# Optimization experiments

Measured on AMD Instinct MI355X. Metric: run time of the kernel, lower is better.

## Reference

```python
import jax, jax.numpy as jnp
import numpy as np

N = 100000   # nodes
E = 1600000  # edges
L = 3        # nlayers
H = 4        # nheads
DH = 32      # nhid (per-head)
F = 128      # nfeat == H*DH (residual-compatible)
NC = 1       # nclass
NEG = 0.2    # leaky relu negative slope (alpha)
EPS = 1e-5   # batchnorm eps


def gat_conv(x, src, dst, W, a_s, a_d, b, concat):
    """PyG-style GATConv (flow=source_to_target): softmax over incoming edges of dst."""
    n = x.shape[0]
    h = (x @ W).reshape(n, a_s.shape[0], a_s.shape[1])  # [N,H,Dh]
    s = jnp.einsum('nhd,hd->nh', h, a_s)  # score from source features
    d = jnp.einsum('nhd,hd->nh', h, a_d)  # score from target features
    e = jax.nn.leaky_relu(s[src] + d[dst], NEG)  # [E,H]
    m = jax.ops.segment_max(e, dst, num_segments=n)
    m = jnp.where(jnp.isfinite(m), m, 0.0)  # nodes with no in-edges
    p = jnp.exp(e - m[dst])
    z = jax.ops.segment_sum(p, dst, num_segments=n)
    alpha = p / (z[dst] + 1e-16)  # [E,H] segment softmax
    out = jax.ops.segment_sum(h[src] * alpha[:, :, None], dst, num_segments=n)  # [N,H,Dh]
    if concat:
        return out.reshape(n, -1) + b
    return out.mean(axis=1) + b


def setup_inputs() -> dict:
    key = jax.random.key(0)
    k = jax.random.split(key, 10)
    return {
        'x': jax.random.normal(k[0], (N, F), jnp.float32),
        'edge_index': jax.random.randint(k[1], (2, E), 0, N, jnp.int32),
        'W': jax.random.normal(k[2], (L, F, H * DH), jnp.float32) * 0.05,
        'att_src': jax.random.normal(k[3], (L, H, DH), jnp.float32) * 0.05,
        'att_dst': jax.random.normal(k[4], (L, H, DH), jnp.float32) * 0.05,
        'bias': jnp.zeros((L, H * DH), jnp.float32),
        'bn_gamma': jnp.ones((L, H * DH), jnp.float32),
        'bn_beta': jnp.zeros((L, H * DH), jnp.float32),
        'bn_mean': jnp.zeros((L, H * DH), jnp.float32),
        'bn_var': jnp.ones((L, H * DH), jnp.float32),
        'W_out': jax.random.normal(k[5], (H * DH, NC), jnp.float32) * 0.05,
        'att_src_out': jax.random.normal(k[6], (1, NC), jnp.float32) * 0.05,
        'att_dst_out': jax.random.normal(k[7], (1, NC), jnp.float32) * 0.05,
        'bias_out': jnp.zeros((NC,), jnp.float32),
    }


def reference(x, edge_index, W, att_src, att_dst, bias, bn_gamma, bn_beta,
              bn_mean, bn_var, W_out, att_src_out, att_dst_out, bias_out):
    src, dst = edge_index[0], edge_index[1]
    h = x  # eval mode: dropout is identity
    for l in range(L):
        res = h
        out = gat_conv(h, src, dst, W[l], att_src[l], att_dst[l], bias[l], concat=True)
        # BatchNorm1d (eval: running stats)
        out = bn_gamma[l] * (out - bn_mean[l]) * jax.lax.rsqrt(bn_var[l] + EPS) + bn_beta[l]
        if l > 0:
            out = out + res
        h = jax.nn.elu(out)
    return gat_conv(h, src, dst, W_out, att_src_out, att_dst_out, bias_out, concat=False)
```

## Files before the change

kernel.cpp:

```cpp
#include <hip/hip_runtime.h>
#include <math.h>

#define NN 100000
#define EE 1600000
#define HH 4
#define LREL 0.2f
#define BNEPS 1e-5f
#define LOG2E 1.4426950408889634f

__global__ void k_zero(int* __restrict__ p, int n) {
    int stride = gridDim.x * blockDim.x;
    for (int i = blockIdx.x * blockDim.x + threadIdx.x; i < n; i += stride) p[i] = 0;
}

__global__ void k_hist(const int* __restrict__ dst, int* __restrict__ deg) {
    int stride = gridDim.x * blockDim.x;
    for (int e = blockIdx.x * blockDim.x + threadIdx.x; e < EE; e += stride)
        atomicAdd(&deg[dst[e]], 1);
}

__global__ void k_scan1(const int* __restrict__ deg, int* __restrict__ rp, int* __restrict__ part) {
    __shared__ int sd[256];
    int i = blockIdx.x * 256 + threadIdx.x;
    int v = (i < NN) ? deg[i] : 0;
    sd[threadIdx.x] = v;
    __syncthreads();
    for (int o = 1; o < 256; o <<= 1) {
        int t = (threadIdx.x >= o) ? sd[threadIdx.x - o] : 0;
        __syncthreads();
        sd[threadIdx.x] += t;
        __syncthreads();
    }
    if (i < NN) rp[i + 1] = sd[threadIdx.x];
    if (threadIdx.x == 255) part[blockIdx.x] = sd[255];
}

__global__ void k_scan2(int* __restrict__ part, int nb) {
    __shared__ int sd[512];
    int v = (threadIdx.x < nb) ? part[threadIdx.x] : 0;
    sd[threadIdx.x] = v;
    __syncthreads();
    for (int o = 1; o < 512; o <<= 1) {
        int t = (threadIdx.x >= o) ? sd[threadIdx.x - o] : 0;
        __syncthreads();
        sd[threadIdx.x] += t;
        __syncthreads();
    }
    if (threadIdx.x < nb) part[threadIdx.x] = sd[threadIdx.x] - v;
}

__global__ void k_scan3(const int* __restrict__ deg, int* __restrict__ rp,
                        const int* __restrict__ part, int* __restrict__ cur) {
    int i = blockIdx.x * 256 + threadIdx.x;
    if (i < NN) {
        int incl = rp[i + 1] + part[blockIdx.x];
        rp[i + 1] = incl;
        cur[i] = incl - deg[i];
        if (i == 0) rp[0] = 0;
    }
}

__global__ void k_scatter(const int* __restrict__ src, const int* __restrict__ dst,
                          int* __restrict__ cur, int* __restrict__ csr) {
    int stride = gridDim.x * blockDim.x;
    for (int e = blockIdx.x * blockDim.x + threadIdx.x; e < EE; e += stride) {
        int p = atomicAdd(&cur[dst[e]], 1);
        csr[p] = src[e];
    }
}

__global__ void k_bnprep(const float* __restrict__ bias, const float* __restrict__ gam,
                         const float* __restrict__ bet, const float* __restrict__ mu,
                         const float* __restrict__ var, float* __restrict__ sc,
                         float* __restrict__ off) {
    int i = threadIdx.x;
    if (i < 384) {
        float rs = rsqrtf(var[i] + BNEPS);
        float s = gam[i] * rs;
        sc[i] = s;
        off[i] = (bias[i] - mu[i]) * s + bet[i];
    }
}

__device__ inline unsigned bf16rne(float f) {
    unsigned u = __float_as_uint(f);
    return (u + 0x7FFFu + ((u >> 16) & 1u)) >> 16;
}

__launch_bounds__(256)
__global__ void k_gemm(const float* __restrict__ x, const float* __restrict__ W,
                       const float* __restrict__ as_, const float* __restrict__ ad_,
                       unsigned* __restrict__ hpb, float* __restrict__ s_arr, float* __restrict__ d_arr) {
    __shared__ float wl[32][128];
    __shared__ float xt[32][68];
    int tid = threadIdx.x;
    int tr = tid >> 5, tc = tid & 31;
    int n0 = blockIdx.x * 64;
    float acc[8][4];
#pragma unroll
    for (int r = 0; r < 8; r++)
#pragma unroll
        for (int c = 0; c < 4; c++) acc[r][c] = 0.f;

    for (int kc = 0; kc < 4; kc++) {
        int k0 = kc * 32;
#pragma unroll
        for (int i = 0; i < 4; i++) {
            int idx = tid + i * 256;
            int r = idx >> 5, c4 = idx & 31;
            *(float4*)&wl[r][c4 * 4] = *(const float4*)&W[(k0 + r) * 128 + c4 * 4];
        }
#pragma unroll
        for (int i = 0; i < 2; i++) {
            int idx = tid + i * 256;
            int r = idx >> 3, c4 = idx & 7;
            int row = n0 + r;
            float4 v = make_float4(0.f, 0.f, 0.f, 0.f);
            if (row < NN) v = *(const float4*)&x[row * 128 + k0 + c4 * 4];
            xt[c4 * 4 + 0][r] = v.x;
            xt[c4 * 4 + 1][r] = v.y;
            xt[c4 * 4 + 2][r] = v.z;
            xt[c4 * 4 + 3][r] = v.w;
        }
        __syncthreads();
#pragma unroll 8
        for (int k = 0; k < 32; k++) {
            float4 w4 = *(float4*)&wl[k][tc * 4];
            float xv[8];
            *(float4*)&xv[0] = *(float4*)&xt[k][tr * 8];
            *(float4*)&xv[4] = *(float4*)&xt[k][tr * 8 + 4];
#pragma unroll
            for (int r = 0; r < 8; r++) {
                acc[r][0] = fmaf(xv[r], w4.x, acc[r][0]);
                acc[r][1] = fmaf(xv[r], w4.y, acc[r][1]);
                acc[r][2] = fmaf(xv[r], w4.z, acc[r][2]);
                acc[r][3] = fmaf(xv[r], w4.w, acc[r][3]);
            }
        }
        __syncthreads();
    }
    int head = tc >> 3;
    float4 a4 = *(const float4*)&as_[head * 32 + (tc & 7) * 4];
    float4 b4 = *(const float4*)&ad_[head * 32 + (tc & 7) * 4];
#pragma unroll
    for (int r = 0; r < 8; r++) {
        int row = n0 + tr * 8 + r;
        float sp = acc[r][0] * a4.x + acc[r][1] * a4.y + acc[r][2] * a4.z + acc[r][3] * a4.w;
        float dp = acc[r][0] * b4.x + acc[r][1] * b4.y + acc[r][2] * b4.z + acc[r][3] * b4.w;
        sp += __shfl_xor(sp, 1); sp += __shfl_xor(sp, 2); sp += __shfl_xor(sp, 4);
        dp += __shfl_xor(dp, 1); dp += __shfl_xor(dp, 2); dp += __shfl_xor(dp, 4);
        if (row < NN) {
            unsigned u0 = bf16rne(acc[r][0]) | (bf16rne(acc[r][1]) << 16);
            unsigned u1 = bf16rne(acc[r][2]) | (bf16rne(acc[r][3]) << 16);
            *(uint2*)&hpb[(size_t)row * 64 + tc * 2] = make_uint2(u0, u1);
            if ((tc & 7) == 0) {
                s_arr[row * HH + head] = sp * LOG2E;
                d_arr[row * HH + head] = dp * LOG2E;
            }
        }
    }
}

__launch_bounds__(256)
__global__ void k_agg(const unsigned* __restrict__ hpb, const float* __restrict__ s_arr,
                      const float* __restrict__ d_arr, const int* __restrict__ rp,
                      const int* __restrict__ csr, const float* __restrict__ scp,
                      const float* __restrict__ offp, const float* __restrict__ hin,
                      float* __restrict__ hout, int use_res) {
    int n = blockIdx.x * 4 + (threadIdx.x >> 6);
    if (n >= NN) return;
    int lane = threadIdx.x & 63;
    int c0 = lane * 2;
    int head = lane >> 4;
    float dn = d_arr[n * HH + head];
    int e0 = rp[n], e1 = rp[n + 1];
    e0 = __builtin_amdgcn_readfirstlane(e0);
    e1 = __builtin_amdgcn_readfirstlane(e1);
    float z = 0.f, a0 = 0.f, a1 = 0.f;
#pragma unroll 8
    for (int j = e0; j < e1; j++) {
        int sid = __builtin_amdgcn_readfirstlane(csr[j]);
        float sv = s_arr[sid * HH + head];
        unsigned u = hpb[(size_t)sid * 64 + lane];
        float e = sv + dn;
        e = fmaxf(e, LREL * e);
        float p = exp2f(e);
        float vx = __uint_as_float(u << 16);
        float vy = __uint_as_float(u & 0xFFFF0000u);
        z += p;
        a0 = fmaf(p, vx, a0);
        a1 = fmaf(p, vy, a1);
    }
    float inv = 1.f / (z + 1e-16f);
    float2 scv = *(const float2*)&scp[c0];
    float2 ofv = *(const float2*)&offp[c0];
    float o0 = fmaf(a0 * inv, scv.x, ofv.x);
    float o1 = fmaf(a1 * inv, scv.y, ofv.y);
    if (use_res) {
        float2 rr = *(const float2*)&hin[n * 128 + c0];
        o0 += rr.x;
        o1 += rr.y;
    }
    o0 = (o0 > 0.f) ? o0 : (__expf(o0) - 1.f);
    o1 = (o1 > 0.f) ? o1 : (__expf(o1) - 1.f);
    *(float2*)&hout[n * 128 + c0] = make_float2(o0, o1);
}

__global__ void k_gemm_out(const float* __restrict__ h, const float* __restrict__ Wo,
                           const float* __restrict__ aso, const float* __restrict__ ado,
                           float2* __restrict__ hos, float* __restrict__ dro) {
    int t = blockIdx.x * 256 + threadIdx.x;
    int n = t >> 2, li = t & 3;
    if (n >= NN) return;
    const float* xr = h + n * 128 + li * 32;
    const float* wr = Wo + li * 32;
    float acc = 0.f;
#pragma unroll
    for (int j = 0; j < 32; j += 4) {
        float4 a = *(const float4*)&xr[j];
        float4 b = *(const float4*)&wr[j];
        acc += a.x * b.x + a.y * b.y + a.z * b.z + a.w * b.w;
    }
    acc += __shfl_xor(acc, 1);
    acc += __shfl_xor(acc, 2);
    if (li == 0) {
        hos[n] = make_float2(acc, acc * aso[0] * LOG2E);
        dro[n] = acc * ado[0] * LOG2E;
    }
}

__global__ void k_agg_out(const float2* __restrict__ hos, const float* __restrict__ dro,
                          const int* __restrict__ rp, const int* __restrict__ csr,
                          const float* __restrict__ bo, float* __restrict__ out) {
    int t = blockIdx.x * 256 + threadIdx.x;
    int n = t >> 3, li = t & 7;
    if (n >= NN) return;
    float dn = dro[n];
    float z = 0.f, a = 0.f;
    int e0 = rp[n], e1 = rp[n + 1];
    for (int j = e0 + li; j < e1; j += 8) {
        int sid = csr[j];
        float2 hs = hos[sid];
        float e = hs.y + dn;
        e = fmaxf(e, LREL * e);
        float p = exp2f(e);
        z += p;
        a = fmaf(p, hs.x, a);
    }
    z += __shfl_xor(z, 1); z += __shfl_xor(z, 2); z += __shfl_xor(z, 4);
    a += __shfl_xor(a, 1); a += __shfl_xor(a, 2); a += __shfl_xor(a, 4);
    if (li == 0) out[n] = a / (z + 1e-16f) + bo[0];
}

extern "C" void kernel_launch(void* const* d_in, const int* in_sizes, int n_in,
                              void* d_out, int out_size, void* d_ws, size_t ws_size,
                              hipStream_t stream) {
    const float* x   = (const float*)d_in[0];
    const int*   ei  = (const int*)d_in[1];
    const float* W   = (const float*)d_in[2];
    const float* as_ = (const float*)d_in[3];
    const float* ad_ = (const float*)d_in[4];
    const float* bias = (const float*)d_in[5];
    const float* gam = (const float*)d_in[6];
    const float* bet = (const float*)d_in[7];
    const float* mu  = (const float*)d_in[8];
    const float* var = (const float*)d_in[9];
    const float* Wo  = (const float*)d_in[10];
    const float* aso = (const float*)d_in[11];
    const float* ado = (const float*)d_in[12];
    const float* bo  = (const float*)d_in[13];
    float* out = (float*)d_out;

    const int* src = ei;
    const int* dst = ei + EE;

    char* wsp = (char*)d_ws;
    size_t off = 0;
    auto alloc = [&](size_t bytes) {
        void* p = wsp + off;
        off += (bytes + 511) & ~(size_t)511;
        return p;
    };
    float* hA     = (float*)alloc((size_t)NN * 128 * 4);
    float* hB     = (float*)alloc((size_t)NN * 128 * 4);
    unsigned* hpb = (unsigned*)alloc((size_t)NN * 64 * 4);
    float* s_arr  = (float*)alloc((size_t)NN * HH * 4);
    float* d_arr  = (float*)alloc((size_t)NN * HH * 4);
    float2* hos   = (float2*)alloc((size_t)NN * 8);
    float* dro    = (float*)alloc((size_t)NN * 4);
    float* bnsc   = (float*)alloc(384 * 4);
    float* bnoff  = (float*)alloc(384 * 4);
    int* deg      = (int*)alloc((size_t)NN * 4);
    int* rp       = (int*)alloc((size_t)(NN + 1) * 4);
    int* cur      = (int*)alloc((size_t)NN * 4);
    int* part     = (int*)alloc(512 * 4);
    int* csr      = (int*)alloc((size_t)EE * 4);

    const int NB = (NN + 255) / 256;

    k_zero<<<512, 256, 0, stream>>>(deg, NN);
    k_hist<<<2048, 256, 0, stream>>>(dst, deg);
    k_scan1<<<NB, 256, 0, stream>>>(deg, rp, part);
    k_scan2<<<1, 512, 0, stream>>>(part, NB);
    k_scan3<<<NB, 256, 0, stream>>>(deg, rp, part, cur);
    k_scatter<<<2048, 256, 0, stream>>>(src, dst, cur, csr);
    k_bnprep<<<1, 384, 0, stream>>>(bias, gam, bet, mu, var, bnsc, bnoff);

    const float* hcur = x;
    const int GEMM_GRID = (NN + 63) / 64;
    const int AGG_GRID = (NN + 3) / 4;
    const int QGRID = (NN * 4 + 255) / 256;
    for (int l = 0; l < 3; l++) {
        k_gemm<<<GEMM_GRID, 256, 0, stream>>>(hcur, W + (size_t)l * 128 * 128,
                                              as_ + l * 128, ad_ + l * 128,
                                              hpb, s_arr, d_arr);
        float* hnext = (l == 1) ? hB : hA;
        k_agg<<<AGG_GRID, 256, 0, stream>>>(hpb, s_arr, d_arr, rp, csr,
                                            bnsc + l * 128, bnoff + l * 128,
                                            hcur, hnext, (l > 0) ? 1 : 0);
        hcur = hnext;
    }
    k_gemm_out<<<QGRID, 256, 0, stream>>>(hcur, Wo, aso, ado, hos, dro);
    k_agg_out<<<(NN * 8 + 255) / 256, 256, 0, stream>>>(hos, dro, rp, csr, bo, out);
}
```

Measured before the change: 848.6 us.

## Build CSR via two-level bucket partition instead of global atomic histogram and scatter

Replaces the per-node global-atomic degree histogram, three-kernel scan and atomic scatter with a bucketed counting sort. Edges are first binned into 512-node buckets using shared-memory histograms and partitioned into a temporary (src,dst) buffer. Each bucket is then sorted locally in shared memory to produce row pointers and CSR. This cuts contended global atomics and random writes, and makes CSR writes local to each bucket. The cost is an extra 8-byte-per-edge buffer pass, and in-bucket edge order becomes nondeterministic.

```diff
diff --git a/kernel.cpp b/kernel.cpp
--- a/kernel.cpp
+++ b/kernel.cpp
@@ -7,65 +7,101 @@
 #define LREL 0.2f
 #define BNEPS 1e-5f
 #define LOG2E 1.4426950408889634f
+#define NBUK 196
+#define PCH 4096
 
 __global__ void k_zero(int* __restrict__ p, int n) {
     int stride = gridDim.x * blockDim.x;
     for (int i = blockIdx.x * blockDim.x + threadIdx.x; i < n; i += stride) p[i] = 0;
 }
 
-__global__ void k_hist(const int* __restrict__ dst, int* __restrict__ deg) {
-    int stride = gridDim.x * blockDim.x;
-    for (int e = blockIdx.x * blockDim.x + threadIdx.x; e < EE; e += stride)
-        atomicAdd(&deg[dst[e]], 1);
-}
-
-__global__ void k_scan1(const int* __restrict__ deg, int* __restrict__ rp, int* __restrict__ part) {
+__global__ void k_bhist(const int* __restrict__ dst, int* __restrict__ bh) {
+    __shared__ int lh[NBUK];
+    int tid = threadIdx.x;
+    for (int i = tid; i < NBUK; i += 256) lh[i] = 0;
+    __syncthreads();
+    int stride = gridDim.x * 256;
+    for (int e = blockIdx.x * 256 + tid; e < EE; e += stride)
+        atomicAdd(&lh[dst[e] >> 9], 1);
+    __syncthreads();
+    for (int i = tid; i < NBUK; i += 256)
+        if (lh[i]) atomicAdd(&bh[i], lh[i]);
+}
+
+__global__ void k_bscan(const int* __restrict__ bh, int* __restrict__ bo, int* __restrict__ bcur) {
     __shared__ int sd[256];
-    int i = blockIdx.x * 256 + threadIdx.x;
-    int v = (i < NN) ? deg[i] : 0;
-    sd[threadIdx.x] = v;
+    int t = threadIdx.x;
+    int v = (t < NBUK) ? bh[t] : 0;
+    sd[t] = v;
     __syncthreads();
     for (int o = 1; o < 256; o <<= 1) {
-        int t = (threadIdx.x >= o) ? sd[threadIdx.x - o] : 0;
-        __syncthreads();
-        sd[threadIdx.x] += t;
-        __syncthreads();
-    }
-    if (i < NN) rp[i + 1] = sd[threadIdx.x];
-    if (threadIdx.x == 255) part[blockIdx.x] = sd[255];
-}
-
-__global__ void k_scan2(int* __restrict__ part, int nb) {
-    __shared__ int sd[512];
-    int v = (threadIdx.x < nb) ? part[threadIdx.x] : 0;
-    sd[threadIdx.x] = v;
-    __syncthreads();
-    for (int o = 1; o < 512; o <<= 1) {
-        int t = (threadIdx.x >= o) ? sd[threadIdx.x - o] : 0;
-        __syncthreads();
-        sd[threadIdx.x] += t;
-        __syncthreads();
-    }
-    if (threadIdx.x < nb) part[threadIdx.x] = sd[threadIdx.x] - v;
-}
-
-__global__ void k_scan3(const int* __restrict__ deg, int* __restrict__ rp,
-                        const int* __restrict__ part, int* __restrict__ cur) {
-    int i = blockIdx.x * 256 + threadIdx.x;
-    if (i < NN) {
-        int incl = rp[i + 1] + part[blockIdx.x];
-        rp[i + 1] = incl;
-        cur[i] = incl - deg[i];
-        if (i == 0) rp[0] = 0;
-    }
-}
-
-__global__ void k_scatter(const int* __restrict__ src, const int* __restrict__ dst,
-                          int* __restrict__ cur, int* __restrict__ csr) {
-    int stride = gridDim.x * blockDim.x;
-    for (int e = blockIdx.x * blockDim.x + threadIdx.x; e < EE; e += stride) {
-        int p = atomicAdd(&cur[dst[e]], 1);
-        csr[p] = src[e];
+        int tv = (t >= o) ? sd[t - o] : 0;
+        __syncthreads();
+        sd[t] += tv;
+        __syncthreads();
+    }
+    int excl = sd[t] - v;
+    if (t < NBUK) { bo[t] = excl; bcur[t] = excl; }
+    if (t == NBUK - 1) bo[NBUK] = excl + v;
+}
+
+__global__ void k_bpart(const int* __restrict__ src, const int* __restrict__ dst,
+                        int* __restrict__ bcur, uint2* __restrict__ ebuf) {
+    __shared__ int lh[NBUK];
+    __shared__ int lcur[NBUK];
+    int tid = threadIdx.x;
+    int e0 = blockIdx.x * PCH, e1 = min(EE, e0 + PCH);
+    for (int i = tid; i < NBUK; i += 256) lh[i] = 0;
+    __syncthreads();
+    for (int e = e0 + tid; e < e1; e += 256)
+        atomicAdd(&lh[dst[e] >> 9], 1);
+    __syncthreads();
+    for (int i = tid; i < NBUK; i += 256)
+        lcur[i] = lh[i] ? atomicAdd(&bcur[i], lh[i]) : 0;
+    __syncthreads();
+    for (int e = e0 + tid; e < e1; e += 256) {
+        int d = dst[e];
+        int b = d >> 9;
+        int p = atomicAdd(&lcur[b], 1);
+        ebuf[p] = make_uint2((unsigned)src[e], (unsigned)d);
+    }
+}
+
+__global__ void k_bfinal(const uint2* __restrict__ ebuf, const int* __restrict__ bo,
+                         int* __restrict__ rp, int* __restrict__ csr) {
+    __shared__ int ldeg[512];
+    __shared__ int lcur2[512];
+    __shared__ int ps[256];
+    int b = blockIdx.x, tid = threadIdx.x;
+    int nbase = b << 9;
+    int e0 = bo[b], e1 = bo[b + 1];
+    ldeg[tid] = 0; ldeg[tid + 256] = 0;
+    __syncthreads();
+    for (int j = e0 + tid; j < e1; j += 256)
+        atomicAdd(&ldeg[ebuf[j].y & 511], 1);
+    __syncthreads();
+    int s0 = ldeg[2 * tid], s1 = ldeg[2 * tid + 1];
+    ps[tid] = s0 + s1;
+    __syncthreads();
+    for (int o = 1; o < 256; o <<= 1) {
+        int tv = (tid >= o) ? ps[tid - o] : 0;
+        __syncthreads();
+        ps[tid] += tv;
+        __syncthreads();
+    }
+    int pex = ps[tid] - (s0 + s1);
+    lcur2[2 * tid] = pex;
+    lcur2[2 * tid + 1] = pex + s0;
+    int n0 = nbase + 2 * tid, n1 = n0 + 1;
+    if (n0 < NN) rp[n0] = e0 + pex;
+    if (n1 < NN) rp[n1] = e0 + pex + s0;
+    if (b == 0 && tid == 0) rp[NN] = EE;
+    __syncthreads();
+    for (int j = e0 + tid; j < e1; j += 256) {
+        uint2 u = ebuf[j];
+        int lid = u.y & 511;
+        int r = atomicAdd(&lcur2[lid], 1);
+        csr[e0 + r] = (int)u.x;
     }
 }
 
@@ -231,7 +267,7 @@
 
 __global__ void k_agg_out(const float2* __restrict__ hos, const float* __restrict__ dro,
                           const int* __restrict__ rp, const int* __restrict__ csr,
-                          const float* __restrict__ bo, float* __restrict__ out) {
+                          const float* __restrict__ bo_, float* __restrict__ out) {
     int t = blockIdx.x * 256 + threadIdx.x;
     int n = t >> 3, li = t & 7;
     if (n >= NN) return;
@@ -249,7 +285,7 @@
     }
     z += __shfl_xor(z, 1); z += __shfl_xor(z, 2); z += __shfl_xor(z, 4);
     a += __shfl_xor(a, 1); a += __shfl_xor(a, 2); a += __shfl_xor(a, 4);
-    if (li == 0) out[n] = a / (z + 1e-16f) + bo[0];
+    if (li == 0) out[n] = a / (z + 1e-16f) + bo_[0];
 }
 
 extern "C" void kernel_launch(void* const* d_in, const int* in_sizes, int n_in,
@@ -268,7 +304,7 @@
     const float* Wo  = (const float*)d_in[10];
     const float* aso = (const float*)d_in[11];
     const float* ado = (const float*)d_in[12];
-    const float* bo  = (const float*)d_in[13];
+    const float* bo_in = (const float*)d_in[13];
     float* out = (float*)d_out;
 
     const int* src = ei;
@@ -290,20 +326,18 @@
     float* dro    = (float*)alloc((size_t)NN * 4);
     float* bnsc   = (float*)alloc(384 * 4);
     float* bnoff  = (float*)alloc(384 * 4);
-    int* deg      = (int*)alloc((size_t)NN * 4);
+    int* bh       = (int*)alloc(NBUK * 4);
+    int* bo       = (int*)alloc((NBUK + 1) * 4);
+    int* bcur     = (int*)alloc(NBUK * 4);
     int* rp       = (int*)alloc((size_t)(NN + 1) * 4);
-    int* cur      = (int*)alloc((size_t)NN * 4);
-    int* part     = (int*)alloc(512 * 4);
+    uint2* ebuf   = (uint2*)alloc((size_t)EE * 8);
     int* csr      = (int*)alloc((size_t)EE * 4);
 
-    const int NB = (NN + 255) / 256;
-
-    k_zero<<<512, 256, 0, stream>>>(deg, NN);
-    k_hist<<<2048, 256, 0, stream>>>(dst, deg);
-    k_scan1<<<NB, 256, 0, stream>>>(deg, rp, part);
-    k_scan2<<<1, 512, 0, stream>>>(part, NB);
-    k_scan3<<<NB, 256, 0, stream>>>(deg, rp, part, cur);
-    k_scatter<<<2048, 256, 0, stream>>>(src, dst, cur, csr);
+    k_zero<<<1, 256, 0, stream>>>(bh, NBUK);
+    k_bhist<<<784, 256, 0, stream>>>(dst, bh);
+    k_bscan<<<1, 256, 0, stream>>>(bh, bo, bcur);
+    k_bpart<<<(EE + PCH - 1) / PCH, 256, 0, stream>>>(src, dst, bcur, ebuf);
+    k_bfinal<<<NBUK, 256, 0, stream>>>(ebuf, bo, rp, csr);
     k_bnprep<<<1, 384, 0, stream>>>(bias, gam, bet, mu, var, bnsc, bnoff);
 
     const float* hcur = x;
@@ -321,5 +355,5 @@
         hcur = hnext;
     }
     k_gemm_out<<<QGRID, 256, 0, stream>>>(hcur, Wo, aso, ado, hos, dro);
-    k_agg_out<<<(NN * 8 + 255) / 256, 256, 0, stream>>>(hos, dro, rp, csr, bo, out);
-}
+    k_agg_out<<<(NN * 8 + 255) / 256, 256, 0, stream>>>(hos, dro, rp, csr, bo_in, out);
+}
```

Result: faster. 725.5 us (-14.5%).
